# Kernel optimization log

Hardware: AMD Instinct MI355X
Metric: run time of the kernel (lower is better)

## Reference

```python
import jax, jax.numpy as jnp
import numpy as np

E_LAYERS, D_MODEL, D_STATE, D_CONV, DT_RANK, D_FF = 2, 512, 16, 2, 32, 2048
BATCH, SEQ = 16, 512


def layer_norm(x, w, b, eps=1e-5):
    m = x.mean(-1, keepdims=True)
    v = ((x - m) ** 2).mean(-1, keepdims=True)
    return (x - m) / jnp.sqrt(v + eps) * w + b


def mamba(x, in_w, conv_w, conv_b, xproj_w, dt_w, dt_b, A_log, D_skip, out_w):
    # x: [B, L, D]; expand=1 so d_inner == D
    Bsz, L, D = x.shape
    N = A_log.shape[-1]
    R = dt_w.shape[-1]
    xz = x @ in_w.T                      # [B, L, 2D]
    xi, z = jnp.split(xz, 2, axis=-1)
    # causal depthwise conv1d, kernel K
    K = conv_w.shape[-1]
    xp = jnp.pad(xi.transpose(0, 2, 1), ((0, 0), (0, 0), (K - 1, 0)))  # [B, D, L+K-1]
    xc = jax.lax.conv_general_dilated(
        xp, conv_w[:, None, :], (1,), 'VALID',
        dimension_numbers=('NCH', 'OIH', 'NCH'), feature_group_count=D)  # [B, D, L]
    xc = jax.nn.silu(xc.transpose(0, 2, 1) + conv_b)                     # [B, L, D]
    proj = xc @ xproj_w.T                                                # [B, L, R+2N]
    dt, Bm, Cm = jnp.split(proj, [R, R + N], axis=-1)
    dt = jax.nn.softplus(dt @ dt_w.T + dt_b)                             # [B, L, D]
    A = -jnp.exp(A_log)                                                  # [D, N]
    dA = jnp.exp(dt[..., None] * A)                                      # [B, L, D, N]
    dBu = dt[..., None] * Bm[:, :, None, :] * xc[..., None]              # [B, L, D, N]

    def step(h, inp):
        a, b = inp
        h = a * h + b
        return h, h

    _, hs = jax.lax.scan(step, jnp.zeros((Bsz, D, N), x.dtype),
                         (dA.transpose(1, 0, 2, 3), dBu.transpose(1, 0, 2, 3)))
    y = jnp.einsum('lbdn,bln->bld', hs, Cm) + D_skip * xc
    return (y * jax.nn.silu(z)) @ out_w.T


def reference(x, in_w, conv_w, conv_b, xproj_w, dt_w, dt_b, A_log, D_skip, out_w,
              ffn1_w, ffn1_b, ffn2_w, ffn2_b, n1_w, n1_b, n2_w, n2_b, fn_w, fn_b):
    E = in_w.shape[0]
    for e in range(E):
        fwd = mamba(x, in_w[e, 0], conv_w[e, 0], conv_b[e, 0], xproj_w[e, 0],
                    dt_w[e, 0], dt_b[e, 0], A_log[e, 0], D_skip[e, 0], out_w[e, 0])
        xr = jnp.flip(x, axis=1)
        rev = mamba(xr, in_w[e, 1], conv_w[e, 1], conv_b[e, 1], xproj_w[e, 1],
                    dt_w[e, 1], dt_b[e, 1], A_log[e, 1], D_skip[e, 1], out_w[e, 1])
        x = x + fwd + jnp.flip(rev, axis=1)
        x = layer_norm(x, n1_w[e], n1_b[e])
        y = jax.nn.gelu(x @ ffn1_w[e].T + ffn1_b[e], approximate=False)
        y = y @ ffn2_w[e].T + ffn2_b[e]
        x = layer_norm(x + y, n2_w[e], n2_b[e])
    return layer_norm(x, fn_w, fn_b)


def setup_inputs() -> dict:
    key = jax.random.key(0)
    E, D, N, K, R, F = E_LAYERS, D_MODEL, D_STATE, D_CONV, DT_RANK, D_FF
    B, L = BATCH, SEQ
    ks = jax.random.split(key, 12)

    def rn(k, shape, s=0.02):
        return jax.random.normal(k, shape, jnp.float32) * s

    A_log = jnp.tile(jnp.log(jnp.arange(1, N + 1, dtype=jnp.float32)), (E, 2, D, 1))
    return {
        'x': jax.random.normal(ks[0], (B, L, D), jnp.float32),
        'in_w': rn(ks[1], (E, 2, 2 * D, D)),
        'conv_w': rn(ks[2], (E, 2, D, K), 0.5),
        'conv_b': jnp.zeros((E, 2, D), jnp.float32),
        'xproj_w': rn(ks[3], (E, 2, R + 2 * N, D)),
        'dt_w': rn(ks[4], (E, 2, D, R), 0.1),
        'dt_b': rn(ks[5], (E, 2, D), 0.1),
        'A_log': A_log,
        'D_skip': jnp.ones((E, 2, D), jnp.float32),
        'out_w': rn(ks[6], (E, 2, D, D)),
        'ffn1_w': rn(ks[7], (E, F, D)),
        'ffn1_b': jnp.zeros((E, F), jnp.float32),
        'ffn2_w': rn(ks[8], (E, D, F)),
        'ffn2_b': jnp.zeros((E, D), jnp.float32),
        'n1_w': jnp.ones((E, D), jnp.float32),
        'n1_b': jnp.zeros((E, D), jnp.float32),
        'n2_w': jnp.ones((E, D), jnp.float32),
        'n2_b': jnp.zeros((E, D), jnp.float32),
        'fn_w': jnp.ones((D,), jnp.float32),
        'fn_b': jnp.zeros((D,), jnp.float32),
    }
```

## Files before the change

kernel.cpp:

```cpp
#include <hip/hip_runtime.h>

#define BB 16
#define LL 512
#define DD 512
#define ROWS (BB*LL)

#define W_IN  0
#define W_XP  2097152
#define W_DT  2359296
#define W_OUT 2621440
#define W_FF1 3670016
#define W_FF2 5767168

typedef unsigned short u16;
typedef __attribute__((ext_vector_type(8))) short short8;
typedef __attribute__((ext_vector_type(4))) float f32x4;
typedef __attribute__((ext_vector_type(4))) unsigned short u16x4;

__device__ __forceinline__ float b2f(u16 u) {
    return __uint_as_float(((unsigned int)u) << 16);
}
__device__ __forceinline__ u16 f2b(float f) {
    unsigned int u = __float_as_uint(f);
    u += 0x7FFFu + ((u >> 16) & 1u);
    return (u16)(u >> 16);
}
__device__ __forceinline__ float ld1(const void* p, size_t i, int f32) {
    return f32 ? ((const float*)p)[i] : b2f(((const u16*)p)[i]);
}
__device__ __forceinline__ float bf_elem(uint4 v, int j) {
    unsigned w = ((const unsigned*)&v)[j >> 1];
    return __uint_as_float((j & 1) ? (w & 0xFFFF0000u) : (w << 16));
}
__device__ __forceinline__ float red16(float x) {
    int v = __float_as_int(x);
    x += __int_as_float(__builtin_amdgcn_update_dpp(0, v, 0xB1, 0xF, 0xF, true));
    v = __float_as_int(x);
    x += __int_as_float(__builtin_amdgcn_update_dpp(0, v, 0x4E, 0xF, 0xF, true));
    v = __float_as_int(x);
    x += __int_as_float(__builtin_amdgcn_update_dpp(0, v, 0x141, 0xF, 0xF, true));
    v = __float_as_int(x);
    x += __int_as_float(__builtin_amdgcn_update_dpp(0, v, 0x140, 0xF, 0xF, true));
    return x;
}
__device__ __forceinline__ void gld16(const u16* g, u16* l) {
    __builtin_amdgcn_global_load_lds(
        (const __attribute__((address_space(1))) unsigned int*)g,
        (__attribute__((address_space(3))) unsigned int*)l, 16, 0, 0);
}

__global__ void detect(const u16* __restrict__ x, int* __restrict__ flag)
{
    __shared__ int s;
    if (threadIdx.x == 0) s = 0;
    __syncthreads();
    u16 v = x[2 * threadIdx.x] & 0x7FFFu;
    if ((v & 0x7F80u) >= 0x5000u) atomicOr(&s, 1);
    __syncthreads();
    if (threadIdx.x == 0) *flag = s;
}

__global__ __launch_bounds__(256)
void cvt_all(const void* __restrict__ X, float* __restrict__ acc, u16* __restrict__ cur,
             const void* __restrict__ in_w, const void* __restrict__ f1w,
             const void* __restrict__ f2w, const void* __restrict__ xp,
             const void* __restrict__ dw, const void* __restrict__ ow,
             u16* __restrict__ wbf, const int* __restrict__ flag)
{
    const int f = *flag;
    size_t t = (size_t)blockIdx.x * 256 + threadIdx.x;
    if (t < 4194304) {
        float v = ld1(X, t, f);
        acc[t] = v; cur[t] = f2b(v);
        return;
    }
    t -= 4194304;
    if (t < 2097152) { wbf[W_IN  + t] = f2b(ld1(in_w, t, f)); return; }
    t -= 2097152;
    if (t < 2097152) { wbf[W_FF1 + t] = f2b(ld1(f1w, t, f)); return; }
    t -= 2097152;
    if (t < 2097152) { wbf[W_FF2 + t] = f2b(ld1(f2w, t, f)); return; }
    t -= 2097152;
    if (t < 262144) {
        int i = (int)t;
        int e = i >> 17, r = (i >> 10) & 127, c = i & 1023;
        int dir = r >> 6, n = r & 63;
        float v = ((c >> 9) == dir)
            ? ld1(xp, ((size_t)(e*2 + dir)*64 + n)*512 + (c & 511), f) : 0.f;
        wbf[W_XP + i] = f2b(v);
        return;
    }
    t -= 262144;
    if (t < 262144) {
        int i = (int)t;
        int e = i >> 17, r = (i >> 7) & 1023, c = i & 127;
        int dir = r >> 9, d = r & 511;
        float v = 0.f;
        if (dir == 0 && c < 32)
            v = ld1(dw, ((size_t)(e*2)*512 + d)*32 + c, f);
        else if (dir == 1 && c >= 64 && c < 96)
            v = ld1(dw, ((size_t)(e*2 + 1)*512 + d)*32 + (c - 64), f);
        wbf[W_DT + i] = f2b(v);
        return;
    }
    t -= 262144;
    {
        int i = (int)t;
        int e = i >> 19, rest = i & 524287;
        int d = rest >> 10, c = rest & 1023;
        int dir = c >> 9;
        wbf[W_OUT + i] = f2b(ld1(ow, ((size_t)(e*2 + dir)*512 + d)*512 + (c & 511), f));
    }
}

__global__ __launch_bounds__(256)
void ksum(const float* __restrict__ psum, u16* __restrict__ proj)
{
    int i = blockIdx.x * 256 + threadIdx.x;
    float s = psum[i] + psum[i + 1048576] + psum[i + 2097152] + psum[i + 3145728];
    proj[i] = f2b(s);
}

__global__ __launch_bounds__(256)
void gemm_mfma(const u16* __restrict__ A, const u16* __restrict__ W,
               float* __restrict__ Cf, u16* __restrict__ Cb, u16* __restrict__ CbT,
               float* __restrict__ Cf2,
               int M, int N, int K,
               const void* __restrict__ bias, size_t boff, int act, int accum,
               int kcnt, const int* __restrict__ flag)
{
    const int f = *flag;
    __shared__ u16 As[128][64];
    __shared__ u16 Ws[128][64];
    const int tid  = threadIdx.x;
    const int lane = tid & 63;
    const int wid  = tid >> 6;
    const int wr   = (wid >> 1) * 64;
    const int wc   = (wid & 1) * 64;
    const int row0 = blockIdx.y * 128;
    const int col0 = blockIdx.x * 128;
    const int mrow = lane & 15;
    const int kq   = (lane >> 4) * 8;
    const int swz  = (mrow & 7) << 3;
    const int kq0  = kq ^ swz;
    const int kq1  = (kq + 32) ^ swz;
    const int srow = wid * 32 + (lane >> 3);
    const int scol = (((lane & 7) ^ (lane >> 3)) & 7) * 8;
    const u16* gA = A + (size_t)(row0 + srow) * K + scol;
    const u16* gW = W + (size_t)(col0 + srow) * K + scol;
    u16* lA = &As[wid * 32][0];
    u16* lW = &Ws[wid * 32][0];
    const int kn = K / kcnt;
    const int kb = blockIdx.z * kn;

    f32x4 acc[4][4] = {};
    for (int k0 = kb; k0 < kb + kn; k0 += 64) {
        #pragma unroll
        for (int q = 0; q < 4; ++q) {
            gld16(gA + k0 + (size_t)(8 * q) * K, lA + 512 * q);
            gld16(gW + k0 + (size_t)(8 * q) * K, lW + 512 * q);
        }
        __syncthreads();
        #pragma unroll
        for (int kk = 0; kk < 2; ++kk) {
            const int kc = kk ? kq1 : kq0;
            short8 af[4], bfr[4];
            #pragma unroll
            for (int mi = 0; mi < 4; ++mi)
                af[mi] = *(const short8*)&As[wr + mi*16 + mrow][kc];
            #pragma unroll
            for (int ni = 0; ni < 4; ++ni)
                bfr[ni] = *(const short8*)&Ws[wc + ni*16 + mrow][kc];
            #pragma unroll
            for (int mi = 0; mi < 4; ++mi)
                #pragma unroll
                for (int ni = 0; ni < 4; ++ni)
                    acc[mi][ni] = __builtin_amdgcn_mfma_f32_16x16x32_bf16(
                        af[mi], bfr[ni], acc[mi][ni], 0, 0, 0);
        }
        __syncthreads();
    }
    const int drow = (lane >> 4) * 4;
    const int dcol = lane & 15;
    if (kcnt > 1 && blockIdx.z > 0 && Cf2) {
        #pragma unroll
        for (int mi = 0; mi < 4; ++mi)
            #pragma unroll
            for (int ni = 0; ni < 4; ++ni) {
                const int rowb = row0 + wr + mi*16 + drow;
                const int col  = col0 + wc + ni*16 + dcol;
                #pragma unroll
                for (int r = 0; r < 4; ++r)
                    Cf2[(size_t)(rowb + r) * N + col] = acc[mi][ni][r];
            }
        return;
    }
    float* Cfz = Cf;
    if (kcnt > 1 && !Cf2) Cfz = Cf + (size_t)blockIdx.z * ((size_t)M * N);
    #pragma unroll
    for (int mi = 0; mi < 4; ++mi) {
        #pragma unroll
        for (int ni = 0; ni < 4; ++ni) {
            const int rowb = row0 + wr + mi*16 + drow;
            const int col  = col0 + wc + ni*16 + dcol;
            float bv = bias ? ld1(bias, boff + col, f) : 0.f;
            float vv[4];
            #pragma unroll
            for (int r = 0; r < 4; ++r) {
                float v = acc[mi][ni][r] + bv;
                if (act == 1) v = (v > 15.f) ? v : log1pf(__expf(v));
                else if (act == 2) v = 0.5f * v * (1.f + erff(v * 0.70710678118f));
                vv[r] = v;
            }
            if (accum) {
                #pragma unroll
                for (int r = 0; r < 4; ++r)
                    Cf[(size_t)(rowb + r) * N + col] += vv[r];
            } else if (Cf) {
                #pragma unroll
                for (int r = 0; r < 4; ++r)
                    Cfz[(size_t)(rowb + r) * N + col] = vv[r];
            } else {
                if (Cb) {
                    #pragma unroll
                    for (int r = 0; r < 4; ++r)
                        Cb[(size_t)(rowb + r) * N + col] = f2b(vv[r]);
                }
                if (CbT) {
                    u16x4 pk;
                    #pragma unroll
                    for (int r = 0; r < 4; ++r) pk[r] = f2b(vv[r]);
                    *(u16x4*)(CbT + (size_t)col * M + rowb) = pk;
                }
            }
        }
    }
}

__global__ __launch_bounds__(256)
void conv_both(u16* __restrict__ xz, const void* __restrict__ cw,
               const void* __restrict__ cb, u16* __restrict__ xc, int e,
               const int* __restrict__ flag)
{
    const int f = *flag;
    int idx = blockIdx.x * 256 + threadIdx.x;
    int row = idx >> 10;
    int c = idx & 1023;
    int dir = c >> 9, d = c & 511;
    int l = row & (LL - 1);
    size_t base = (size_t)row * 2048 + dir * 1024;
    float xcur = b2f(xz[base + d]);
    int dsign = dir ? 1 : -1;
    int ln = l + dsign;
    float xnb = (ln >= 0 && ln < LL) ? b2f(xz[base + dsign*2048 + d]) : 0.f;
    size_t co = (size_t)(e*2 + dir) * 1024 + 2*d;
    float v = ld1(cw, co, f) * xnb + ld1(cw, co + 1, f) * xcur
            + ld1(cb, (size_t)(e*2 + dir)*512 + d, f);
    xc[(size_t)row * 1024 + c] = f2b(v / (1.f + __expf(-v)));
    float z = b2f(xz[base + 512 + d]);
    xz[base + 512 + d] = f2b(z / (1.f + __expf(-z)));
}

__global__ __launch_bounds__(256)
void transp(const u16* __restrict__ src, u16* __restrict__ dst, int C)
{
    __shared__ u16 t[64][72];
    const int c0 = blockIdx.x * 64, r0 = blockIdx.y * 64;
    const int rr = threadIdx.x >> 3, cc = (threadIdx.x & 7) * 8;
    #pragma unroll
    for (int i = 0; i < 2; ++i) {
        uint4 v = *(const uint4*)(src + (size_t)(r0 + rr + i*32) * C + c0 + cc);
        *(uint4*)&t[rr + i*32][cc] = v;
    }
    __syncthreads();
    const int tc = threadIdx.x >> 3, tr = (threadIdx.x & 7) * 8;
    #pragma unroll
    for (int i = 0; i < 2; ++i) {
        u16 tmp[8];
        #pragma unroll
        for (int j = 0; j < 8; ++j) tmp[j] = t[tr + j][tc + i*32];
        *(uint4*)(dst + (size_t)(c0 + tc + i*32) * 8192 + r0 + tr) = *(uint4*)tmp;
    }
}

template<int DIR>
__device__ __forceinline__ void scan_dir(
    const u16* __restrict__ dtp, const u16* __restrict__ xcp,
    const u16* __restrict__ Bp, const u16* __restrict__ Cp,
    const u16* __restrict__ zp, u16* __restrict__ gp,
    float Av, float Dv, int lane)
{
    float h = 0.f;
    int lb = DIR ? (LL - 8) : 0;
    const int stp = DIR ? -8 : 8;
    uint4 d8 = *(const uint4*)(dtp + lb);
    uint4 x8 = *(const uint4*)(xcp + lb);
    uint4 B8 = *(const uint4*)(Bp + lb);
    uint4 C8 = *(const uint4*)(Cp + lb);
    for (int it = 0; it < LL / 8; ++it) {
        const int lbn = lb + stp;
        uint4 nd = d8, nx = x8, nB = B8, nC = C8;
        if (it < LL / 8 - 1) {
            nd = *(const uint4*)(dtp + lbn);
            nx = *(const uint4*)(xcp + lbn);
            nB = *(const uint4*)(Bp + lbn);
            nC = *(const uint4*)(Cp + lbn);
        }
        float keep = 0.f;
        #pragma unroll
        for (int jj = 0; jj < 8; ++jj) {
            const int j = DIR ? (7 - jj) : jj;
            float dtv = bf_elem(d8, j);
            float xv  = bf_elem(x8, j);
            float Bn  = bf_elem(B8, j);
            float Cn  = bf_elem(C8, j);
            h = __expf(dtv * Av) * h + (dtv * xv) * Bn;
            float c = red16(h * Cn) + Dv * xv;
            keep = (lane == j) ? c : keep;
        }
        if (lane < 8) {
            float zs = b2f(zp[(lb + lane) * 2048]);
            gp[(lb + lane) * 1024] = f2b(keep * zs);
        }
        d8 = nd; x8 = nx; B8 = nB; C8 = nC;
        lb = lbn;
    }
}

__global__ __launch_bounds__(256)
void ssm_scan(u16* __restrict__ g, const u16* __restrict__ dtT,
              const u16* __restrict__ xcT, const u16* __restrict__ projT,
              const u16* __restrict__ xz,
              const void* __restrict__ A_log, const void* __restrict__ Dsk,
              int e, const int* __restrict__ flag)
{
    const int f = *flag;
    const int lane = threadIdx.x & 15;
    const int gg = blockIdx.x * 16 + (threadIdx.x >> 4);
    const int dir = gg >> 13;
    const int rem = gg & 8191;
    const int b = rem >> 9, d = rem & 511;
    const int ed = e * 2 + dir;
    const float Av = -__expf(ld1(A_log, (size_t)ed * 8192 + d * 16 + lane, f));
    const float Dv = ld1(Dsk, (size_t)ed * 512 + d, f);
    const int col = dir * 512 + d;
    const size_t tb = (size_t)col * 8192 + b * 512;
    const u16* dtp = dtT + tb;
    const u16* xcp = xcT + tb;
    const u16* Bp  = projT + (size_t)(dir * 64 + 32 + lane) * 8192 + b * 512;
    const u16* Cp  = Bp + (size_t)16 * 8192;
    u16* gp = g + (size_t)b * LL * 1024 + col;
    const u16* zp = xz + (size_t)b * LL * 2048 + dir * 1024 + 512 + d;
    if (dir == 0) scan_dir<0>(dtp, xcp, Bp, Cp, zp, gp, Av, Dv, lane);
    else          scan_dir<1>(dtp, xcp, Bp, Cp, zp, gp, Av, Dv, lane);
}

__global__ __launch_bounds__(256)
void lnorm(const u16* __restrict__ Xb, const float* __restrict__ Xf,
           const float* __restrict__ Xf2,
           const void* __restrict__ w, size_t wo, const void* __restrict__ b, size_t bo,
           void* __restrict__ out, int omode, float* __restrict__ accf,
           const int* __restrict__ flag)
{
    const int f = *flag;
    int wid = (blockIdx.x * 256 + threadIdx.x) >> 6;
    int lane = threadIdx.x & 63;
    size_t base = (size_t)wid * DD;
    float v[8];
    float s = 0.f;
    #pragma unroll
    for (int i = 0; i < 8; ++i) {
        int c = lane + i*64;
        float t = 0.f;
        if (Xb) t += b2f(Xb[base + c]);
        if (Xf) t += Xf[base + c];
        if (Xf2) t += Xf2[base + c];
        v[i] = t; s += t;
    }
    #pragma unroll
    for (int off = 32; off > 0; off >>= 1) s += __shfl_xor(s, off);
    float mean = s * (1.f/512.f);
    float var = 0.f;
    #pragma unroll
    for (int i = 0; i < 8; ++i) { float dlt = v[i] - mean; var += dlt*dlt; }
    #pragma unroll
    for (int off = 32; off > 0; off >>= 1) var += __shfl_xor(var, off);
    float rstd = rsqrtf(var * (1.f/512.f) + 1e-5f);
    #pragma unroll
    for (int i = 0; i < 8; ++i) {
        int c = lane + i*64;
        float o = (v[i] - mean) * rstd * ld1(w, wo + c, f) + ld1(b, bo + c, f);
        if (omode && f) ((float*)out)[base + c] = o;
        else            ((u16*)out)[base + c] = f2b(o);
        if (accf) accf[base + c] = o;
    }
}

extern "C" void kernel_launch(void* const* d_in, const int* in_sizes, int n_in,
                              void* d_out, int out_size, void* d_ws, size_t ws_size,
                              hipStream_t stream)
{
    (void)in_sizes; (void)n_in; (void)out_size; (void)ws_size;
    const void* X       = d_in[0];
    const void* in_w    = d_in[1];
    const void* conv_w  = d_in[2];
    const void* conv_b  = d_in[3];
    const void* xproj_w = d_in[4];
    const void* dt_w    = d_in[5];
    const void* dt_b    = d_in[6];
    const void* A_log   = d_in[7];
    const void* D_skip  = d_in[8];
    const void* out_w   = d_in[9];
    const void* ffn1_w  = d_in[10];
    const void* ffn1_b  = d_in[11];
    const void* ffn2_w  = d_in[12];
    const void* ffn2_b  = d_in[13];
    const void* n1_w    = d_in[14];
    const void* n1_b    = d_in[15];
    const void* n2_w    = d_in[16];
    const void* n2_b    = d_in[17];
    const void* fn_w    = d_in[18];
    const void* fn_b    = d_in[19];

    char* p = (char*)d_ws;
    float* acc   = (float*)(p);
    u16*   cur   = (u16*)(p + 16777216);
    u16*   xz    = (u16*)(p + 25165824);
    u16*   xc    = (u16*)(p + 58720256);
    u16*   dtT   = (u16*)(p + 58720256);
    u16*   g     = (u16*)(p + 75497472);
    u16*   proj  = (u16*)(p + 92274688);
    int*   flag  = (int*)(p + 94371840);
    u16*   wbf   = (u16*)(p + 94375936);
    u16*   xcT   = (u16*)(p + 110104576);
    u16*   projT = (u16*)(p + 126881792);
    u16*   ffh   = xz;
    float* y2    = (float*)xc;
    u16*   x1    = g;
    float* psum  = (float*)g;
    float* psk   = (float*)xcT;

    detect<<<1, 512, 0, stream>>>((const u16*)X, flag);
    cvt_all<<<47104, 256, 0, stream>>>(X, acc, cur, in_w, ffn1_w, ffn2_w,
                                       xproj_w, dt_w, out_w, wbf, flag);

    for (int e = 0; e < 2; ++e) {
        size_t eo = (size_t)e * 512;
        gemm_mfma<<<dim3(16,64), 256, 0, stream>>>(
            cur, wbf + W_IN + (size_t)e*1048576, nullptr, xz, nullptr, nullptr,
            ROWS, 2048, 512, nullptr, 0, 0, 0, 1, flag);
        conv_both<<<ROWS*1024/256, 256, 0, stream>>>(xz, conv_w, conv_b, xc, e, flag);
        transp<<<dim3(16,128), 256, 0, stream>>>(xc, xcT, 1024);
        gemm_mfma<<<dim3(1,64,4), 256, 0, stream>>>(
            xc, wbf + W_XP + (size_t)e*131072, psum, nullptr, nullptr, nullptr,
            ROWS, 128, 1024, nullptr, 0, 0, 0, 4, flag);
        ksum<<<4096, 256, 0, stream>>>(psum, proj);
        transp<<<dim3(2,128), 256, 0, stream>>>(proj, projT, 128);
        gemm_mfma<<<dim3(8,64), 256, 0, stream>>>(
            proj, wbf + W_DT + (size_t)e*131072, nullptr, nullptr, dtT, nullptr,
            ROWS, 1024, 128, dt_b, (size_t)e*1024, 1, 0, 1, flag);
        ssm_scan<<<1024, 256, 0, stream>>>(g, dtT, xcT, projT, xz,
                                           A_log, D_skip, e, flag);
        gemm_mfma<<<dim3(4,64,2), 256, 0, stream>>>(
            g, wbf + W_OUT + (size_t)e*524288, acc, nullptr, nullptr, psk,
            ROWS, 512, 1024, nullptr, 0, 0, 1, 2, flag);
        lnorm<<<2048, 256, 0, stream>>>(nullptr, acc, psk, n1_w, eo, n1_b, eo,
                                        x1, 0, nullptr, flag);
        gemm_mfma<<<dim3(16,64), 256, 0, stream>>>(
            x1, wbf + W_FF1 + (size_t)e*1048576, nullptr, ffh, nullptr, nullptr,
            ROWS, 2048, 512, ffn1_b, (size_t)e*2048, 2, 0, 1, flag);
        gemm_mfma<<<dim3(4,64,2), 256, 0, stream>>>(
            ffh, wbf + W_FF2 + (size_t)e*1048576, y2, nullptr, nullptr, psk,
            ROWS, 512, 2048, ffn2_b, eo, 0, 0, 2, flag);
        lnorm<<<2048, 256, 0, stream>>>(x1, y2, psk, n2_w, eo, n2_b, eo, cur, 0,
                                        (e == 0) ? acc : nullptr, flag);
    }
    lnorm<<<2048, 256, 0, stream>>>(cur, nullptr, nullptr, fn_w, 0, fn_b, 0,
                                    d_out, 1, nullptr, flag);
}
```

Baseline: 1.049 ms.

## Batch scan reductions with transpose-style DPP butterfly and fuse z SiLU into GEMM

The per-timestep 16-lane reduction of h*C inside the selective scan is replaced by a reduce-scatter butterfly across the 8 timesteps of each chunk. Each exchange stage halves the number of live values, so far fewer DPP/swizzle operations and adds are needed per chunk, and lane j ends with the sum for timestep j. Separately, SiLU on the z half is moved into the in-projection GEMM epilogue as a new activation mode, so conv_both no longer reads and rewrites z. The cost is more select instructions and register pressure in the scan, plus a branch on the column in the GEMM epilogue.

```diff
diff --git a/kernel.cpp b/kernel.cpp
--- a/kernel.cpp
+++ b/kernel.cpp
@@ -32,16 +32,14 @@
     unsigned w = ((const unsigned*)&v)[j >> 1];
     return __uint_as_float((j & 1) ? (w & 0xFFFF0000u) : (w << 16));
 }
-__device__ __forceinline__ float red16(float x) {
-    int v = __float_as_int(x);
-    x += __int_as_float(__builtin_amdgcn_update_dpp(0, v, 0xB1, 0xF, 0xF, true));
-    v = __float_as_int(x);
-    x += __int_as_float(__builtin_amdgcn_update_dpp(0, v, 0x4E, 0xF, 0xF, true));
-    v = __float_as_int(x);
-    x += __int_as_float(__builtin_amdgcn_update_dpp(0, v, 0x141, 0xF, 0xF, true));
-    v = __float_as_int(x);
-    x += __int_as_float(__builtin_amdgcn_update_dpp(0, v, 0x140, 0xF, 0xF, true));
-    return x;
+template<int PAT>
+__device__ __forceinline__ float dppx(float x) {
+    return __int_as_float(__builtin_amdgcn_update_dpp(0, __float_as_int(x),
+                                                      PAT, 0xF, 0xF, true));
+}
+template<int OFF>
+__device__ __forceinline__ float swzx(float x) {
+    return __int_as_float(__builtin_amdgcn_ds_swizzle(__float_as_int(x), OFF));
 }
 __device__ __forceinline__ void gld16(const u16* g, u16* l) {
     __builtin_amdgcn_global_load_lds(
@@ -210,6 +208,7 @@
                 float v = acc[mi][ni][r] + bv;
                 if (act == 1) v = (v > 15.f) ? v : log1pf(__expf(v));
                 else if (act == 2) v = 0.5f * v * (1.f + erff(v * 0.70710678118f));
+                else if (act == 3) { if (col & 512) v = v / (1.f + __expf(-v)); }
                 vv[r] = v;
             }
             if (accum) {
@@ -238,7 +237,7 @@
 }
 
 __global__ __launch_bounds__(256)
-void conv_both(u16* __restrict__ xz, const void* __restrict__ cw,
+void conv_both(const u16* __restrict__ xz, const void* __restrict__ cw,
                const void* __restrict__ cb, u16* __restrict__ xc, int e,
                const int* __restrict__ flag)
 {
@@ -257,8 +256,6 @@
     float v = ld1(cw, co, f) * xnb + ld1(cw, co + 1, f) * xcur
             + ld1(cb, (size_t)(e*2 + dir)*512 + d, f);
     xc[(size_t)row * 1024 + c] = f2b(v / (1.f + __expf(-v)));
-    float z = b2f(xz[base + 512 + d]);
-    xz[base + 512 + d] = f2b(z / (1.f + __expf(-z)));
 }
 
 __global__ __launch_bounds__(256)
@@ -293,6 +290,9 @@
     float h = 0.f;
     int lb = DIR ? (LL - 8) : 0;
     const int stp = DIR ? -8 : 8;
+    const bool s0 = (lane & 1) != 0;
+    const bool s1 = (lane & 2) != 0;
+    const bool s2 = (lane & 4) != 0;
     uint4 d8 = *(const uint4*)(dtp + lb);
     uint4 x8 = *(const uint4*)(xcp + lb);
     uint4 B8 = *(const uint4*)(Bp + lb);
@@ -306,7 +306,8 @@
             nB = *(const uint4*)(Bp + lbn);
             nC = *(const uint4*)(Cp + lbn);
         }
-        float keep = 0.f;
+        float y[8];
+        float xsel = 0.f;
         #pragma unroll
         for (int jj = 0; jj < 8; ++jj) {
             const int j = DIR ? (7 - jj) : jj;
@@ -315,12 +316,30 @@
             float Bn  = bf_elem(B8, j);
             float Cn  = bf_elem(C8, j);
             h = __expf(dtv * Av) * h + (dtv * xv) * Bn;
-            float c = red16(h * Cn) + Dv * xv;
-            keep = (lane == j) ? c : keep;
-        }
+            y[j] = h * Cn;
+            xsel = (lane == j) ? xv : xsel;
+        }
+        float z0[4];
+        #pragma unroll
+        for (int m = 0; m < 4; ++m) {
+            float mine = s0 ? y[2*m+1] : y[2*m];
+            float send = s0 ? y[2*m]   : y[2*m+1];
+            z0[m] = mine + dppx<0xB1>(send);
+        }
+        float z1[2];
+        #pragma unroll
+        for (int m = 0; m < 2; ++m) {
+            float mine = s1 ? z0[2*m+1] : z0[2*m];
+            float send = s1 ? z0[2*m]   : z0[2*m+1];
+            z1[m] = mine + dppx<0x4E>(send);
+        }
+        float mine = s2 ? z1[1] : z1[0];
+        float send = s2 ? z1[0] : z1[1];
+        float r = mine + swzx<0x101F>(send);
+        r += swzx<0x201F>(r);
         if (lane < 8) {
             float zs = b2f(zp[(lb + lane) * 2048]);
-            gp[(lb + lane) * 1024] = f2b(keep * zs);
+            gp[(lb + lane) * 1024] = f2b((r + Dv * xsel) * zs);
         }
         d8 = nd; x8 = nx; B8 = nB; C8 = nC;
         lb = lbn;
@@ -448,7 +467,7 @@
         size_t eo = (size_t)e * 512;
         gemm_mfma<<<dim3(16,64), 256, 0, stream>>>(
             cur, wbf + W_IN + (size_t)e*1048576, nullptr, xz, nullptr, nullptr,
-            ROWS, 2048, 512, nullptr, 0, 0, 0, 1, flag);
+            ROWS, 2048, 512, nullptr, 0, 3, 0, 1, flag);
         conv_both<<<ROWS*1024/256, 256, 0, stream>>>(xz, conv_w, conv_b, xc, e, flag);
         transp<<<dim3(16,128), 256, 0, stream>>>(xc, xcT, 1024);
         gemm_mfma<<<dim3(1,64,4), 256, 0, stream>>>(
```

New measurement: 1.067 ms. Within noise of the previous version (+1.8%).
